# Kernel optimization log

Hardware: AMD Instinct MI355X
Metric: run time of the kernel (lower is better)

## Reference

```python
import jax, jax.numpy as jnp
import numpy as np

H, N, CH = 256, 64, 1

def _r2c(x):
    return x[..., 0] + 1j * x[..., 1]

def setup_inputs() -> dict:
    key = jax.random.key(0)
    kA, kB, kC, kdt = jax.random.split(key, 4)
    # Build a Hurwitz A (skew-Hermitian - 0.5*I) so dA = (I-dt/2 A)^-1 (I+dt/2 A) has spectral radius < 1
    M = jax.random.normal(kA, (H, N, N, 2), dtype=jnp.float32) / np.float32(np.sqrt(N))
    Mc = _r2c(M)
    Ac = 0.5 * (Mc - jnp.conjugate(jnp.swapaxes(Mc, -1, -2))) - 0.5 * jnp.eye(N, dtype=Mc.dtype)
    A = jnp.stack([Ac.real, Ac.imag], axis=-1)  # (H,N,N,2)
    B = jax.random.normal(kB, (H, N, 2), dtype=jnp.float32)
    C = jax.random.normal(kC, (CH, H, N, 2), dtype=jnp.float32)
    # log_dt uniform in [log(1e-3), log(1e-1)], shape (H,1) per bilinear docstring
    log_dt = jax.random.uniform(kdt, (H, 1), dtype=jnp.float32,
                                minval=np.float32(np.log(1e-3)), maxval=np.float32(np.log(1e-1)))
    return {"A": A, "B": B, "C": C, "log_dt": log_dt, "L": 2048}

def _bilinear(dt, Ac, Bc):
    # dt: (H,1), Ac: (H,N,N) complex, Bc: (H,N) complex
    n = Ac.shape[-1]
    I = jnp.eye(n, dtype=Ac.dtype)
    half = (dt.astype(Ac.real.dtype) / 2)[:, None]  # (H,1,1)
    A_back = I - half * Ac
    A_fwd = I + half * Ac
    dB = dt.astype(Ac.dtype) * jnp.linalg.solve(A_back, Bc[..., None])[..., 0]  # (H,N)
    dA = jnp.linalg.solve(A_back, A_fwd)  # (H,N,N)
    return dA, dB

def _krylov(L, dA, dB):
    # x[..., l] = dA^l dB via squaring-doubling, matches S4 krylov math
    x = dB[..., None]  # (H,N,1)
    A_ = dA
    while x.shape[-1] < L:
        x = jnp.concatenate([x, jnp.einsum('hnm,hml->hnl', A_, x)], axis=-1)
        A_ = A_ @ A_
    return x[..., :L]

def reference(A, B, C, log_dt, L):
    Ac, Bc, Cc = _r2c(A), _r2c(B), _r2c(C)
    dt = jnp.exp(log_dt)  # (H,1)
    dA, dB = _bilinear(dt, Ac, Bc)
    x = _krylov(L, dA, dB)  # (H,N,L) complex
    # k[c,h,l] = sum_n C[c,h,n] * (dA^l dB)[h,n]; torch .float() on complex keeps real part
    k = jnp.einsum('chn,hnl->chl', Cc, x).real.astype(jnp.float32)
    return k
```

## Files before the change

kernel.cpp:

```cpp
#include <hip/hip_runtime.h>
#include <math.h>

#define NH   256
#define NN   64
#define LSEQ 2048
#define RS   72
#define PSZ  4608
#define GSZ  2304
#define NTH  1024

typedef __attribute__((ext_vector_type(8))) short short8;
typedef __attribute__((ext_vector_type(4))) float float4_t;
typedef unsigned short u16;

#define MFMA(a,b,c) __builtin_amdgcn_mfma_f32_16x16x32_bf16((a),(b),(c),0,0,0)
#define PERM_HI 0x07060302u

static __device__ __forceinline__ void split2(float v, unsigned& hb, unsigned& lb) {
    hb = __float_as_uint(v) & 0xffff0000u;
    lb = __float_as_uint(v - __uint_as_float(hb));
}
static __device__ __forceinline__ float ld2(const u16* hp, const u16* lp, int idx) {
    return __uint_as_float((unsigned)hp[idx] << 16)
         + __uint_as_float((unsigned)lp[idx] << 16);
}

static __device__ __forceinline__ void frag_vals(const unsigned* e, short8& hi, short8& lo) {
    unsigned lb[8];
#pragma unroll
    for (int m = 0; m < 8; ++m) {
        unsigned hv = e[m] & 0xffff0000u;
        lb[m] = __float_as_uint(__uint_as_float(e[m]) - __uint_as_float(hv));
    }
    union { short8 s; unsigned u[4]; } H, L;
#pragma unroll
    for (int m = 0; m < 4; ++m) {
        H.u[m] = __builtin_amdgcn_perm(e[2*m+1],  e[2*m],  PERM_HI);
        L.u[m] = __builtin_amdgcn_perm(lb[2*m+1], lb[2*m], PERM_HI);
    }
    hi = H.s; lo = L.s;
}

template<int ASZ, int BSZ, bool IMAG>
static __device__ __forceinline__ void cmm_tile(
    const u16* __restrict__ Ab, const u16* __restrict__ Bb,
    int arow, int bcol, int fq,
    float4_t& accP, float4_t& accN, float4_t& accI1, float4_t& accI2)
{
#pragma unroll
    for (int ks = 0; ks < 2; ++ks) {
        const int k0 = ks*32 + fq*8;
        const u16* ap = Ab + arow*RS + k0;
        const u16* bp = Bb + bcol*RS + k0;
        short8 Arh = *(const short8*)(ap);
        short8 Arl = *(const short8*)(ap + ASZ);
        short8 Aih = *(const short8*)(ap + 2*ASZ);
        short8 Ail = *(const short8*)(ap + 3*ASZ);
        short8 Brh = *(const short8*)(bp);
        short8 Brl = *(const short8*)(bp + BSZ);
        short8 Bih = *(const short8*)(bp + 2*BSZ);
        short8 Bil = *(const short8*)(bp + 3*BSZ);
        accP = MFMA(Arh, Brh, accP); accP = MFMA(Arh, Brl, accP); accP = MFMA(Arl, Brh, accP);
        accN = MFMA(Aih, Bih, accN); accN = MFMA(Aih, Bil, accN); accN = MFMA(Ail, Bih, accN);
        if (IMAG) {
            accI1 = MFMA(Arh, Bih, accI1); accI1 = MFMA(Arh, Bil, accI1); accI1 = MFMA(Arl, Bih, accI1);
            accI2 = MFMA(Aih, Brh, accI2); accI2 = MFMA(Aih, Brl, accI2); accI2 = MFMA(Ail, Brh, accI2);
        }
    }
}

static __device__ __forceinline__ void store_P_vals(
    u16* XR, u16* XT, int ti, int bcol, int fq,
    const float* p_r, const float* p_i)
{
    unsigned hR[4], lR[4], hI[4], lI[4];
#pragma unroll
    for (int r = 0; r < 4; ++r) {
        split2(p_r[r], hR[r], lR[r]);
        split2(p_i[r], hI[r], lI[r]);
        int row = ti*16 + fq*4 + r;
        XR[row*RS + bcol]         = (u16)(hR[r] >> 16);
        XR[PSZ + row*RS + bcol]   = (u16)(lR[r] >> 16);
        XR[2*PSZ + row*RS + bcol] = (u16)(hI[r] >> 16);
        XR[3*PSZ + row*RS + bcol] = (u16)(lI[r] >> 16);
    }
    int tb = bcol*RS + ti*16 + fq*4;
    uint2 w;
    w.x = __builtin_amdgcn_perm(hR[1], hR[0], PERM_HI);
    w.y = __builtin_amdgcn_perm(hR[3], hR[2], PERM_HI);
    *(uint2*)&XT[tb] = w;
    w.x = __builtin_amdgcn_perm(lR[1], lR[0], PERM_HI);
    w.y = __builtin_amdgcn_perm(lR[3], lR[2], PERM_HI);
    *(uint2*)&XT[PSZ + tb] = w;
    w.x = __builtin_amdgcn_perm(hI[1], hI[0], PERM_HI);
    w.y = __builtin_amdgcn_perm(hI[3], hI[2], PERM_HI);
    *(uint2*)&XT[2*PSZ + tb] = w;
    w.x = __builtin_amdgcn_perm(lI[1], lI[0], PERM_HI);
    w.y = __builtin_amdgcn_perm(lI[3], lI[2], PERM_HI);
    *(uint2*)&XT[3*PSZ + tb] = w;
}

__global__ __launch_bounds__(NTH, 4) void ssm_kernel(
    const float* __restrict__ Ag,
    const float* __restrict__ Bg,
    const float* __restrict__ Cg,
    const float* __restrict__ LogDt,
    float* __restrict__ outp)
{
    __shared__ __align__(16) unsigned char lds[130048];
    u16* XR = (u16*)(lds);
    u16* XT = (u16*)(lds +  36864);
    u16* XF = (u16*)(lds +  73728);
    u16* Gm = (u16*)(lds + 110592);
    float* bvr = (float*)(lds + 129024);
    float* bvi = (float*)(lds + 129280);
    float* urr = (float*)(lds + 129536);
    float* uri = (float*)(lds + 129792);

    const int t    = threadIdx.x;
    const int lane = t & 63;
    const int wv   = t >> 6;
    const int ti   = wv >> 2, tj = wv & 3;
    const int fm   = lane & 15, fq = lane >> 4;
    const int h    = blockIdx.x;

    const float dt  = expf(LogDt[h]);
    const float hdt = 0.5f * dt;

    const float2* A2 = (const float2*)(Ag + (size_t)h * NN * NN * 2);
    const float4_t z4 = {0.f, 0.f, 0.f, 0.f};

#pragma unroll
    for (int e = 0; e < 4; ++e) {
        int idx = t + e*NTH;
        int i = idx >> 6, j = idx & 63;
        float2 a = A2[idx];
        unsigned hb, lb;
        split2((i == j ? 1.0f : 0.0f) + hdt * a.x, hb, lb);
        XR[i*RS + j]       = (u16)(hb >> 16);
        XR[PSZ + i*RS + j] = (u16)(lb >> 16);
        XT[j*RS + i]       = (u16)(hb >> 16);
        XT[PSZ + j*RS + i] = (u16)(lb >> 16);
        split2(hdt * a.y, hb, lb);
        XR[2*PSZ + i*RS + j] = (u16)(hb >> 16);
        XR[3*PSZ + i*RS + j] = (u16)(lb >> 16);
        XT[2*PSZ + j*RS + i] = (u16)(hb >> 16);
        XT[3*PSZ + j*RS + i] = (u16)(lb >> 16);
    }
    if (t < NN) {
        float2 bv = ((const float2*)Bg)[h*NN + t];
        float2 cv = ((const float2*)Cg)[h*NN + t];
        bvr[t] = bv.x; bvi[t] = bv.y;
        unsigned hb, lb;
        split2(cv.x, hb, lb);
        Gm[t]       = (u16)(hb >> 16);
        Gm[GSZ + t] = (u16)(lb >> 16);
        split2(cv.y, hb, lb);
        Gm[2*GSZ + t] = (u16)(hb >> 16);
        Gm[3*GSZ + t] = (u16)(lb >> 16);
    }
    __syncthreads();

    const int arow = ti*16 + fm;
    const int bcol = tj*16 + fm;

    {
        float4_t aP = z4, aN = z4, aI1 = z4, aI2 = z4;
#pragma unroll
        for (int ks = 0; ks < 2; ++ks) {
            const int k0 = ks*32 + fq*8;
            unsigned vr[8], vi[8];
#pragma unroll
            for (int j = 0; j < 8; ++j) {
                float2 a = A2[arow*NN + k0 + j];
                vr[j] = __float_as_uint((arow == k0 + j ? 1.0f : 0.0f) - hdt * a.x);
                vi[j] = __float_as_uint(-hdt * a.y);
            }
            short8 Arh, Arl, Aih, Ail;
            frag_vals(vr, Arh, Arl);
            frag_vals(vi, Aih, Ail);
            const u16* bp = XT + bcol*RS + k0;
            short8 Brh = *(const short8*)(bp);
            short8 Brl = *(const short8*)(bp + PSZ);
            short8 Bih = *(const short8*)(bp + 2*PSZ);
            short8 Bil = *(const short8*)(bp + 3*PSZ);
            aP = MFMA(Arh, Brh, aP); aP = MFMA(Arh, Brl, aP); aP = MFMA(Arl, Brh, aP);
            aN = MFMA(Aih, Bih, aN); aN = MFMA(Aih, Bil, aN); aN = MFMA(Ail, Bih, aN);
            aI1 = MFMA(Arh, Bih, aI1); aI1 = MFMA(Arh, Bil, aI1); aI1 = MFMA(Arl, Bih, aI1);
            aI2 = MFMA(Aih, Brh, aI2); aI2 = MFMA(Aih, Brl, aI2); aI2 = MFMA(Ail, Brh, aI2);
        }
#pragma unroll
        for (int rp = 0; rp < 2; ++rp) {
            int row0 = ti*16 + fq*4 + rp*2;
            unsigned h0, l0, h1, l1;
            split2(aP[rp*2]   - aN[rp*2],   h0, l0);
            split2(aP[rp*2+1] - aN[rp*2+1], h1, l1);
            *(unsigned*)&XF[bcol*RS + row0]       = __builtin_amdgcn_perm(h1, h0, PERM_HI);
            *(unsigned*)&XF[PSZ + bcol*RS + row0] = __builtin_amdgcn_perm(l1, l0, PERM_HI);
            split2(aI1[rp*2]   + aI2[rp*2],   h0, l0);
            split2(aI1[rp*2+1] + aI2[rp*2+1], h1, l1);
            *(unsigned*)&XF[2*PSZ + bcol*RS + row0] = __builtin_amdgcn_perm(h1, h0, PERM_HI);
            *(unsigned*)&XF[3*PSZ + bcol*RS + row0] = __builtin_amdgcn_perm(l1, l0, PERM_HI);
        }
    }
    __syncthreads();

    {
        float4_t aP = z4, aN = z4, aI1 = z4, aI2 = z4;
        cmm_tile<PSZ, PSZ, true>(XR, XF, arow, bcol, fq, aP, aN, aI1, aI2);
        __syncthreads();
#pragma unroll
        for (int r = 0; r < 4; ++r) {
            int row = ti*16 + fq*4 + r;
            unsigned hb, lb;
            split2(aP[r] - aN[r], hb, lb);
            XR[row*RS + bcol]       = (u16)(hb >> 16);
            XR[PSZ + row*RS + bcol] = (u16)(lb >> 16);
            split2(aI1[r] + aI2[r], hb, lb);
            XR[2*PSZ + row*RS + bcol] = (u16)(hb >> 16);
            XR[3*PSZ + row*RS + bcol] = (u16)(lb >> 16);
        }
    }
    __syncthreads();

    {
        float4_t aP = z4, aN = z4, aI1 = z4, aI2 = z4;
        cmm_tile<PSZ, PSZ, true>(XR, XF, arow, bcol, fq, aP, aN, aI1, aI2);
        float p_r[4], p_i[4];
#pragma unroll
        for (int r = 0; r < 4; ++r) {
            int row = ti*16 + fq*4 + r;
            float2 a = A2[row*NN + bcol];
            float dd  = (row == bcol ? 1.0f : 0.0f);
            float x1r = dd + hdt * a.x;
            float x1i = hdt * a.y;
            float vvr = ld2(XR, XR + PSZ, row*RS + bcol);
            float vvi = ld2(XR + 2*PSZ, XR + 3*PSZ, row*RS + bcol);
            p_r[r] = 2.0f*(3.0f*x1r - 3.0f*vvr + (aP[r] - aN[r])) - dd;
            p_i[r] = 2.0f*(3.0f*x1i - 3.0f*vvi + (aI1[r] + aI2[r]));
        }
        __syncthreads();
        store_P_vals(XR, XT, ti, bcol, fq, p_r, p_i);
    }
    __syncthreads();

    {
        int n = t >> 4, part = t & 15;
        float ar = 0.f, ai = 0.f;
#pragma unroll
        for (int qq = 0; qq < 4; ++qq) {
            int k = part + 16*qq;
            float mr = ld2(XR, XR + PSZ, n*RS + k);
            float mi = ld2(XR + 2*PSZ, XR + 3*PSZ, n*RS + k);
            ar += mr*bvr[k] - mi*bvi[k];
            ai += mr*bvi[k] + mi*bvr[k];
        }
#pragma unroll
        for (int off = 8; off; off >>= 1) { ar += __shfl_xor(ar, off); ai += __shfl_xor(ai, off); }
        if (part == 0) { urr[n] = ar; uri[n] = ai; }
    }
    __syncthreads();

#pragma unroll 1
    for (int s = 1; s <= 9; ++s) {
        if (s == 1) {
            int n = t >> 4, part = t & 15;
            float ar = 0.f, ai = 0.f;
#pragma unroll
            for (int qq = 0; qq < 4; ++qq) {
                int k = part + 16*qq;
                float mr = ld2(XR, XR + PSZ, n*RS + k);
                float mi = ld2(XR + 2*PSZ, XR + 3*PSZ, n*RS + k);
                ar += mr*urr[k] - mi*uri[k];
                ai += mr*uri[k] + mi*urr[k];
            }
#pragma unroll
            for (int off = 8; off; off >>= 1) { ar += __shfl_xor(ar, off); ai += __shfl_xor(ai, off); }
            if (part == 0) {
                float u_r = urr[n], u_i = uri[n];
                unsigned hb, lb;
                split2(hdt*(u_r + bvr[n]), hb, lb);
                XF[n]       = (u16)(hb >> 16); XF[PSZ + n]       = (u16)(lb >> 16);
                split2(hdt*(u_i + bvi[n]), hb, lb);
                XF[2*PSZ + n] = (u16)(hb >> 16); XF[3*PSZ + n]   = (u16)(lb >> 16);
                split2(hdt*(ar + u_r), hb, lb);
                XF[RS + n]       = (u16)(hb >> 16); XF[PSZ + RS + n]   = (u16)(lb >> 16);
                split2(hdt*(ai + u_i), hb, lb);
                XF[2*PSZ + RS + n] = (u16)(hb >> 16); XF[3*PSZ + RS + n] = (u16)(lb >> 16);
            }
        } else if (s <= 6) {
            const int C = 1 << (s-1);
            const int nT = (s == 6) ? 8 : 4;
            if (wv < nT) {
                const int rt = wv >> 2, ct = wv & 3;
                float4_t aP = z4, aN = z4, aI1 = z4, aI2 = z4;
                cmm_tile<PSZ, PSZ, true>(XF, XR, rt*16 + fm, ct*16 + fm, fq, aP, aN, aI1, aI2);
#pragma unroll
                for (int r = 0; r < 4; ++r) {
                    int orow = C + rt*16 + fq*4 + r;
                    int oc   = ct*16 + fm;
                    unsigned hb, lb;
                    split2(aP[r] - aN[r], hb, lb);
                    XF[orow*RS + oc]       = (u16)(hb >> 16);
                    XF[PSZ + orow*RS + oc] = (u16)(lb >> 16);
                    split2(aI1[r] + aI2[r], hb, lb);
                    XF[2*PSZ + orow*RS + oc] = (u16)(hb >> 16);
                    XF[3*PSZ + orow*RS + oc] = (u16)(lb >> 16);
                }
            }
        } else {
            const int C = 1 << (s-7);
            if (wv < 4) {
                float4_t aP = z4, aN = z4, aI1 = z4, aI2 = z4;
                cmm_tile<GSZ, PSZ, true>(Gm, XT, fm, wv*16 + fm, fq, aP, aN, aI1, aI2);
#pragma unroll
                for (int r = 0; r < 4; ++r) {
                    int orow = C + fq*4 + r;
                    int oc   = wv*16 + fm;
                    unsigned hb, lb;
                    split2(aP[r] - aN[r], hb, lb);
                    Gm[orow*RS + oc]       = (u16)(hb >> 16);
                    Gm[GSZ + orow*RS + oc] = (u16)(lb >> 16);
                    split2(aI1[r] + aI2[r], hb, lb);
                    Gm[2*GSZ + orow*RS + oc] = (u16)(hb >> 16);
                    Gm[3*GSZ + orow*RS + oc] = (u16)(lb >> 16);
                }
            }
        }
        float4_t sP = z4, sN = z4, sI1 = z4, sI2 = z4;
        cmm_tile<PSZ, PSZ, true>(XR, XT, arow, bcol, fq, sP, sN, sI1, sI2);
        __syncthreads();
        float p_r[4], p_i[4];
#pragma unroll
        for (int r = 0; r < 4; ++r) { p_r[r] = sP[r] - sN[r]; p_i[r] = sI1[r] + sI2[r]; }
        store_P_vals(XR, XT, ti, bcol, fq, p_r, p_i);
        __syncthreads();
    }

#pragma unroll 1
    for (int tt = 0; tt < 4; ++tt) {
        if (tt < 3 && wv < 4) {
            const int ab = tt * 8;
            float4_t aP = z4, aN = z4, aI1 = z4, aI2 = z4;
            cmm_tile<GSZ, PSZ, true>(Gm, XT, ab + fm, wv*16 + fm, fq, aP, aN, aI1, aI2);
#pragma unroll
            for (int r = 0; r < 4; ++r) {
                int orow = 8 + ab + fq*4 + r;
                if (orow < 32) {
                    int oc = wv*16 + fm;
                    unsigned hb, lb;
                    split2(aP[r] - aN[r], hb, lb);
                    Gm[orow*RS + oc]       = (u16)(hb >> 16);
                    Gm[GSZ + orow*RS + oc] = (u16)(lb >> 16);
                    split2(aI1[r] + aI2[r], hb, lb);
                    Gm[2*GSZ + orow*RS + oc] = (u16)(hb >> 16);
                    Gm[3*GSZ + orow*RS + oc] = (u16)(lb >> 16);
                }
            }
        }
        if (wv >= 4 && wv < 8) {
            const int jb = tt * 8;
            int ga = jb + fm; if (ga > 31) ga = 31;
            float4_t aP = z4, aN = z4, aI1 = z4, aI2 = z4;
            cmm_tile<GSZ, PSZ, false>(Gm, XF, ga, (wv-4)*16 + fm, fq, aP, aN, aI1, aI2);
            if (fq < 2) {
                size_t base = (size_t)h * LSEQ;
#pragma unroll
                for (int r = 0; r < 4; ++r)
                    outp[base + (jb + fq*4 + r)*NN + (wv-4)*16 + fm] = aP[r] - aN[r];
            }
        }
        if (tt < 3) __syncthreads();
    }
}

extern "C" void kernel_launch(void* const* d_in, const int* in_sizes, int n_in,
                              void* d_out, int out_size, void* d_ws, size_t ws_size,
                              hipStream_t stream) {
    const float* A  = (const float*)d_in[0];
    const float* B  = (const float*)d_in[1];
    const float* C  = (const float*)d_in[2];
    const float* ld = (const float*)d_in[3];
    float* out = (float*)d_out;
    ssm_kernel<<<dim3(NH), dim3(NTH), 0, stream>>>(A, B, C, ld, out);
}
```

Baseline: 99.89 us.

## Split waves: half compute paired squaring tiles, half run Krylov steps concurrently

The 64x64 complex matrix squaring now uses only waves 0-7, each computing two 16x16 output tiles that share the A fragment, instead of all 16 waves computing one tile each. Waves 8-15 take over the Krylov extension and Gm work and run it concurrently with the squaring rather than serially before it. The aim is to reuse A-operand LDS loads and overlap the two independent chains inside each step. In exchange each squaring wave has twice the work and uses more accumulator registers, and the diff leaves in a dead dummy load.

```diff
diff --git a/kernel.cpp b/kernel.cpp
--- a/kernel.cpp
+++ b/kernel.cpp
@@ -69,6 +69,51 @@
     }
 }
 
+template<int ASZ, int BSZ>
+static __device__ __forceinline__ void cmm_pair(
+    const u16* __restrict__ Ab, const u16* __restrict__ Bb,
+    int arow, int bcol0, int fq,
+    float4_t& P0, float4_t& N0, float4_t& I10, float4_t& I20,
+    float4_t& P1, float4_t& N1, float4_t& I11, float4_t& I21)
+{
+#pragma unroll
+    for (int ks = 0; ks < 2; ++ks) {
+        const int k0 = ks*32 + fq*8;
+        const u16* ap = Ab + arow*RS + k0;
+        short8 Arh = *(const short8*)(ap);
+        short8 Arl = *(const short8*)(ap + ASZ);
+        short8 Aih = *(const short8*)(ap + 2*ASZ);
+        short8 Ail = *(const short8*)(ap + 3*ASZ);
+        const u16* bp0 = Bb + bcol0*RS + k0;
+        {
+            short8 Brh = *(const short8*)(bp0);
+            short8 Brl = *(const short8*)(bp0 + BSZ);
+            short8 Bih = *(const short8*)(bp0 + 2*BSZ);
+            short8 Bil = *(const short8*)(bp0 + 3*BSZ);
+            P0 = MFMA(Arh, Brh, P0); P0 = MFMA(Arh, Brl, P0); P0 = MFMA(Arl, Brh, P0);
+            N0 = MFMA(Aih, Bih, N0); N0 = MFMA(Aih, Bil, N0); N0 = MFMA(Ail, Bih, N0);
+            I10 = MFMA(Arh, Bih, I10); I10 = MFMA(Arh, Bil, I10); I10 = MFMA(Arl, Bih, I10);
+            I20 = MFMA(Aih, Brh, I20); I20 = MFMA(Aih, Brl, I20); I20 = MFMA(Ail, Brh, I20);
+        }
+        {
+            const u16* bp1 = bp0 + 16;
+            short8 Brh = *(const short8*)(bp1 + 16*(RS/16)*0 + (RS*16 - 16) + 16 - RS*16 + RS*16);
+            (void)Brh;
+        }
+        {
+            const u16* bp1 = Bb + (bcol0 + 16)*RS + k0;
+            short8 Brh = *(const short8*)(bp1);
+            short8 Brl = *(const short8*)(bp1 + BSZ);
+            short8 Bih = *(const short8*)(bp1 + 2*BSZ);
+            short8 Bil = *(const short8*)(bp1 + 3*BSZ);
+            P1 = MFMA(Arh, Brh, P1); P1 = MFMA(Arh, Brl, P1); P1 = MFMA(Arl, Brh, P1);
+            N1 = MFMA(Aih, Bih, N1); N1 = MFMA(Aih, Bil, N1); N1 = MFMA(Ail, Bih, N1);
+            I11 = MFMA(Arh, Bih, I11); I11 = MFMA(Arh, Bil, I11); I11 = MFMA(Arl, Bih, I11);
+            I21 = MFMA(Aih, Brh, I21); I21 = MFMA(Aih, Brl, I21); I21 = MFMA(Ail, Brh, I21);
+        }
+    }
+}
+
 static __device__ __forceinline__ void store_P_vals(
     u16* XR, u16* XT, int ti, int bcol, int fq,
     const float* p_r, const float* p_i)
@@ -120,9 +165,13 @@
     const int t    = threadIdx.x;
     const int lane = t & 63;
     const int wv   = t >> 6;
-    const int ti   = wv >> 2, tj = wv & 3;
     const int fm   = lane & 15, fq = lane >> 4;
     const int h    = blockIdx.x;
+
+    const int tip  = wv >> 1, tjp = wv & 1;
+    const int parow = tip*16 + fm;
+    const int pb0   = tjp*32 + fm;
+    const int pb1   = pb0 + 16;
 
     const float dt  = expf(LogDt[h]);
     const float hdt = 0.5f * dt;
@@ -161,86 +210,117 @@
     }
     __syncthreads();
 
-    const int arow = ti*16 + fm;
-    const int bcol = tj*16 + fm;
-
-    {
-        float4_t aP = z4, aN = z4, aI1 = z4, aI2 = z4;
+    if (wv < 8) {
+        float4_t P0 = z4, N0 = z4, I10 = z4, I20 = z4;
+        float4_t P1 = z4, N1 = z4, I11 = z4, I21 = z4;
 #pragma unroll
         for (int ks = 0; ks < 2; ++ks) {
             const int k0 = ks*32 + fq*8;
             unsigned vr[8], vi[8];
 #pragma unroll
             for (int j = 0; j < 8; ++j) {
-                float2 a = A2[arow*NN + k0 + j];
-                vr[j] = __float_as_uint((arow == k0 + j ? 1.0f : 0.0f) - hdt * a.x);
+                float2 a = A2[parow*NN + k0 + j];
+                vr[j] = __float_as_uint((parow == k0 + j ? 1.0f : 0.0f) - hdt * a.x);
                 vi[j] = __float_as_uint(-hdt * a.y);
             }
             short8 Arh, Arl, Aih, Ail;
             frag_vals(vr, Arh, Arl);
             frag_vals(vi, Aih, Ail);
-            const u16* bp = XT + bcol*RS + k0;
-            short8 Brh = *(const short8*)(bp);
-            short8 Brl = *(const short8*)(bp + PSZ);
-            short8 Bih = *(const short8*)(bp + 2*PSZ);
-            short8 Bil = *(const short8*)(bp + 3*PSZ);
-            aP = MFMA(Arh, Brh, aP); aP = MFMA(Arh, Brl, aP); aP = MFMA(Arl, Brh, aP);
-            aN = MFMA(Aih, Bih, aN); aN = MFMA(Aih, Bil, aN); aN = MFMA(Ail, Bih, aN);
-            aI1 = MFMA(Arh, Bih, aI1); aI1 = MFMA(Arh, Bil, aI1); aI1 = MFMA(Arl, Bih, aI1);
-            aI2 = MFMA(Aih, Brh, aI2); aI2 = MFMA(Aih, Brl, aI2); aI2 = MFMA(Ail, Brh, aI2);
-        }
-#pragma unroll
-        for (int rp = 0; rp < 2; ++rp) {
-            int row0 = ti*16 + fq*4 + rp*2;
-            unsigned h0, l0, h1, l1;
-            split2(aP[rp*2]   - aN[rp*2],   h0, l0);
-            split2(aP[rp*2+1] - aN[rp*2+1], h1, l1);
-            *(unsigned*)&XF[bcol*RS + row0]       = __builtin_amdgcn_perm(h1, h0, PERM_HI);
-            *(unsigned*)&XF[PSZ + bcol*RS + row0] = __builtin_amdgcn_perm(l1, l0, PERM_HI);
-            split2(aI1[rp*2]   + aI2[rp*2],   h0, l0);
-            split2(aI1[rp*2+1] + aI2[rp*2+1], h1, l1);
-            *(unsigned*)&XF[2*PSZ + bcol*RS + row0] = __builtin_amdgcn_perm(h1, h0, PERM_HI);
-            *(unsigned*)&XF[3*PSZ + bcol*RS + row0] = __builtin_amdgcn_perm(l1, l0, PERM_HI);
+#pragma unroll
+            for (int p = 0; p < 2; ++p) {
+                const u16* bp = XT + (pb0 + p*16)*RS + k0;
+                short8 Brh = *(const short8*)(bp);
+                short8 Brl = *(const short8*)(bp + PSZ);
+                short8 Bih = *(const short8*)(bp + 2*PSZ);
+                short8 Bil = *(const short8*)(bp + 3*PSZ);
+                float4_t &aP = p ? P1 : P0, &aN = p ? N1 : N0;
+                float4_t &aI1 = p ? I11 : I10, &aI2 = p ? I21 : I20;
+                aP = MFMA(Arh, Brh, aP); aP = MFMA(Arh, Brl, aP); aP = MFMA(Arl, Brh, aP);
+                aN = MFMA(Aih, Bih, aN); aN = MFMA(Aih, Bil, aN); aN = MFMA(Ail, Bih, aN);
+                aI1 = MFMA(Arh, Bih, aI1); aI1 = MFMA(Arh, Bil, aI1); aI1 = MFMA(Arl, Bih, aI1);
+                aI2 = MFMA(Aih, Brh, aI2); aI2 = MFMA(Aih, Brl, aI2); aI2 = MFMA(Ail, Brh, aI2);
+            }
+        }
+#pragma unroll
+        for (int p = 0; p < 2; ++p) {
+            const int bcol = pb0 + p*16;
+            const float4_t &aP = p ? P1 : P0, &aN = p ? N1 : N0;
+            const float4_t &aI1 = p ? I11 : I10, &aI2 = p ? I21 : I20;
+#pragma unroll
+            for (int rp = 0; rp < 2; ++rp) {
+                int row0 = tip*16 + fq*4 + rp*2;
+                unsigned h0, l0, h1, l1;
+                split2(aP[rp*2]   - aN[rp*2],   h0, l0);
+                split2(aP[rp*2+1] - aN[rp*2+1], h1, l1);
+                *(unsigned*)&XF[bcol*RS + row0]       = __builtin_amdgcn_perm(h1, h0, PERM_HI);
+                *(unsigned*)&XF[PSZ + bcol*RS + row0] = __builtin_amdgcn_perm(l1, l0, PERM_HI);
+                split2(aI1[rp*2]   + aI2[rp*2],   h0, l0);
+                split2(aI1[rp*2+1] + aI2[rp*2+1], h1, l1);
+                *(unsigned*)&XF[2*PSZ + bcol*RS + row0] = __builtin_amdgcn_perm(h1, h0, PERM_HI);
+                *(unsigned*)&XF[3*PSZ + bcol*RS + row0] = __builtin_amdgcn_perm(l1, l0, PERM_HI);
+            }
         }
     }
     __syncthreads();
 
     {
-        float4_t aP = z4, aN = z4, aI1 = z4, aI2 = z4;
-        cmm_tile<PSZ, PSZ, true>(XR, XF, arow, bcol, fq, aP, aN, aI1, aI2);
+        float4_t P0 = z4, N0 = z4, I10 = z4, I20 = z4;
+        float4_t P1 = z4, N1 = z4, I11 = z4, I21 = z4;
+        if (wv < 8)
+            cmm_pair<PSZ, PSZ>(XR, XF, parow, pb0, fq, P0, N0, I10, I20, P1, N1, I11, I21);
         __syncthreads();
-#pragma unroll
-        for (int r = 0; r < 4; ++r) {
-            int row = ti*16 + fq*4 + r;
-            unsigned hb, lb;
-            split2(aP[r] - aN[r], hb, lb);
-            XR[row*RS + bcol]       = (u16)(hb >> 16);
-            XR[PSZ + row*RS + bcol] = (u16)(lb >> 16);
-            split2(aI1[r] + aI2[r], hb, lb);
-            XR[2*PSZ + row*RS + bcol] = (u16)(hb >> 16);
-            XR[3*PSZ + row*RS + bcol] = (u16)(lb >> 16);
+        if (wv < 8) {
+#pragma unroll
+            for (int p = 0; p < 2; ++p) {
+                const int bcol = pb0 + p*16;
+                const float4_t &aP = p ? P1 : P0, &aN = p ? N1 : N0;
+                const float4_t &aI1 = p ? I11 : I10, &aI2 = p ? I21 : I20;
+#pragma unroll
+                for (int r = 0; r < 4; ++r) {
+                    int row = tip*16 + fq*4 + r;
+                    unsigned hb, lb;
+                    split2(aP[r] - aN[r], hb, lb);
+                    XR[row*RS + bcol]       = (u16)(hb >> 16);
+                    XR[PSZ + row*RS + bcol] = (u16)(lb >> 16);
+                    split2(aI1[r] + aI2[r], hb, lb);
+                    XR[2*PSZ + row*RS + bcol] = (u16)(hb >> 16);
+                    XR[3*PSZ + row*RS + bcol] = (u16)(lb >> 16);
+                }
+            }
         }
     }
     __syncthreads();
 
     {
-        float4_t aP = z4, aN = z4, aI1 = z4, aI2 = z4;
-        cmm_tile<PSZ, PSZ, true>(XR, XF, arow, bcol, fq, aP, aN, aI1, aI2);
-        float p_r[4], p_i[4];
-#pragma unroll
-        for (int r = 0; r < 4; ++r) {
-            int row = ti*16 + fq*4 + r;
-            float2 a = A2[row*NN + bcol];
-            float dd  = (row == bcol ? 1.0f : 0.0f);
-            float x1r = dd + hdt * a.x;
-            float x1i = hdt * a.y;
-            float vvr = ld2(XR, XR + PSZ, row*RS + bcol);
-            float vvi = ld2(XR + 2*PSZ, XR + 3*PSZ, row*RS + bcol);
-            p_r[r] = 2.0f*(3.0f*x1r - 3.0f*vvr + (aP[r] - aN[r])) - dd;
-            p_i[r] = 2.0f*(3.0f*x1i - 3.0f*vvi + (aI1[r] + aI2[r]));
+        float p_r[2][4], p_i[2][4];
+        if (wv < 8) {
+            float4_t P0 = z4, N0 = z4, I10 = z4, I20 = z4;
+            float4_t P1 = z4, N1 = z4, I11 = z4, I21 = z4;
+            cmm_pair<PSZ, PSZ>(XR, XF, parow, pb0, fq, P0, N0, I10, I20, P1, N1, I11, I21);
+#pragma unroll
+            for (int p = 0; p < 2; ++p) {
+                const int bcol = pb0 + p*16;
+                const float4_t &aP = p ? P1 : P0, &aN = p ? N1 : N0;
+                const float4_t &aI1 = p ? I11 : I10, &aI2 = p ? I21 : I20;
+#pragma unroll
+                for (int r = 0; r < 4; ++r) {
+                    int row = tip*16 + fq*4 + r;
+                    float2 a = A2[row*NN + bcol];
+                    float dd  = (row == bcol ? 1.0f : 0.0f);
+                    float x1r = dd + hdt * a.x;
+                    float x1i = hdt * a.y;
+                    float vvr = ld2(XR, XR + PSZ, row*RS + bcol);
+                    float vvi = ld2(XR + 2*PSZ, XR + 3*PSZ, row*RS + bcol);
+                    p_r[p][r] = 2.0f*(3.0f*x1r - 3.0f*vvr + (aP[r] - aN[r])) - dd;
+                    p_i[p][r] = 2.0f*(3.0f*x1i - 3.0f*vvi + (aI1[r] + aI2[r]));
+                }
+            }
         }
         __syncthreads();
-        store_P_vals(XR, XT, ti, bcol, fq, p_r, p_i);
+        if (wv < 8) {
+            store_P_vals(XR, XT, tip, pb0, fq, p_r[0], p_i[0]);
+            store_P_vals(XR, XT, tip, pb1, fq, p_r[1], p_i[1]);
+        }
     }
     __syncthreads();
 
@@ -263,77 +343,88 @@
 
 #pragma unroll 1
     for (int s = 1; s <= 9; ++s) {
-        if (s == 1) {
-            int n = t >> 4, part = t & 15;
-            float ar = 0.f, ai = 0.f;
-#pragma unroll
-            for (int qq = 0; qq < 4; ++qq) {
-                int k = part + 16*qq;
-                float mr = ld2(XR, XR + PSZ, n*RS + k);
-                float mi = ld2(XR + 2*PSZ, XR + 3*PSZ, n*RS + k);
-                ar += mr*urr[k] - mi*uri[k];
-                ai += mr*uri[k] + mi*urr[k];
-            }
-#pragma unroll
-            for (int off = 8; off; off >>= 1) { ar += __shfl_xor(ar, off); ai += __shfl_xor(ai, off); }
-            if (part == 0) {
-                float u_r = urr[n], u_i = uri[n];
-                unsigned hb, lb;
-                split2(hdt*(u_r + bvr[n]), hb, lb);
-                XF[n]       = (u16)(hb >> 16); XF[PSZ + n]       = (u16)(lb >> 16);
-                split2(hdt*(u_i + bvi[n]), hb, lb);
-                XF[2*PSZ + n] = (u16)(hb >> 16); XF[3*PSZ + n]   = (u16)(lb >> 16);
-                split2(hdt*(ar + u_r), hb, lb);
-                XF[RS + n]       = (u16)(hb >> 16); XF[PSZ + RS + n]   = (u16)(lb >> 16);
-                split2(hdt*(ai + u_i), hb, lb);
-                XF[2*PSZ + RS + n] = (u16)(hb >> 16); XF[3*PSZ + RS + n] = (u16)(lb >> 16);
-            }
-        } else if (s <= 6) {
-            const int C = 1 << (s-1);
-            const int nT = (s == 6) ? 8 : 4;
-            if (wv < nT) {
-                const int rt = wv >> 2, ct = wv & 3;
-                float4_t aP = z4, aN = z4, aI1 = z4, aI2 = z4;
-                cmm_tile<PSZ, PSZ, true>(XF, XR, rt*16 + fm, ct*16 + fm, fq, aP, aN, aI1, aI2);
-#pragma unroll
-                for (int r = 0; r < 4; ++r) {
-                    int orow = C + rt*16 + fq*4 + r;
-                    int oc   = ct*16 + fm;
+        float4_t P0 = z4, N0 = z4, I10 = z4, I20 = z4;
+        float4_t P1 = z4, N1 = z4, I11 = z4, I21 = z4;
+        if (wv >= 8) {
+            if (s == 1) {
+                int n = (t >> 3) & 63, part = t & 7;
+                float ar = 0.f, ai = 0.f;
+#pragma unroll
+                for (int qq = 0; qq < 8; ++qq) {
+                    int k = part + 8*qq;
+                    float mr = ld2(XR, XR + PSZ, n*RS + k);
+                    float mi = ld2(XR + 2*PSZ, XR + 3*PSZ, n*RS + k);
+                    ar += mr*urr[k] - mi*uri[k];
+                    ai += mr*uri[k] + mi*urr[k];
+                }
+#pragma unroll
+                for (int off = 4; off; off >>= 1) { ar += __shfl_xor(ar, off); ai += __shfl_xor(ai, off); }
+                if (part == 0) {
+                    float u_r = urr[n], u_i = uri[n];
                     unsigned hb, lb;
-                    split2(aP[r] - aN[r], hb, lb);
-                    XF[orow*RS + oc]       = (u16)(hb >> 16);
-                    XF[PSZ + orow*RS + oc] = (u16)(lb >> 16);
-                    split2(aI1[r] + aI2[r], hb, lb);
-                    XF[2*PSZ + orow*RS + oc] = (u16)(hb >> 16);
-                    XF[3*PSZ + orow*RS + oc] = (u16)(lb >> 16);
+                    split2(hdt*(u_r + bvr[n]), hb, lb);
+                    XF[n]       = (u16)(hb >> 16); XF[PSZ + n]       = (u16)(lb >> 16);
+                    split2(hdt*(u_i + bvi[n]), hb, lb);
+                    XF[2*PSZ + n] = (u16)(hb >> 16); XF[3*PSZ + n]   = (u16)(lb >> 16);
+                    split2(hdt*(ar + u_r), hb, lb);
+                    XF[RS + n]       = (u16)(hb >> 16); XF[PSZ + RS + n]   = (u16)(lb >> 16);
+                    split2(hdt*(ai + u_i), hb, lb);
+                    XF[2*PSZ + RS + n] = (u16)(hb >> 16); XF[3*PSZ + RS + n] = (u16)(lb >> 16);
+                }
+            } else if (s <= 6) {
+                const int C = 1 << (s-1);
+                const int w = wv - 8;
+                const int nT = (s == 6) ? 8 : 4;
+                if (w < nT) {
+                    const int rt = w >> 2, ct = w & 3;
+                    float4_t aP = z4, aN = z4, aI1 = z4, aI2 = z4;
+                    cmm_tile<PSZ, PSZ, true>(XF, XR, rt*16 + fm, ct*16 + fm, fq, aP, aN, aI1, aI2);
+#pragma unroll
+                    for (int r = 0; r < 4; ++r) {
+                        int orow = C + rt*16 + fq*4 + r;
+                        int oc   = ct*16 + fm;
+                        unsigned hb, lb;
+                        split2(aP[r] - aN[r], hb, lb);
+                        XF[orow*RS + oc]       = (u16)(hb >> 16);
+                        XF[PSZ + orow*RS + oc] = (u16)(lb >> 16);
+                        split2(aI1[r] + aI2[r], hb, lb);
+                        XF[2*PSZ + orow*RS + oc] = (u16)(hb >> 16);
+                        XF[3*PSZ + orow*RS + oc] = (u16)(lb >> 16);
+                    }
+                }
+            } else {
+                const int C = 1 << (s-7);
+                const int w = wv - 8;
+                if (w < 4) {
+                    float4_t aP = z4, aN = z4, aI1 = z4, aI2 = z4;
+                    cmm_tile<GSZ, PSZ, true>(Gm, XT, fm, w*16 + fm, fq, aP, aN, aI1, aI2);
+#pragma unroll
+                    for (int r = 0; r < 4; ++r) {
+                        int orow = C + fq*4 + r;
+                        int oc   = w*16 + fm;
+                        unsigned hb, lb;
+                        split2(aP[r] - aN[r], hb, lb);
+                        Gm[orow*RS + oc]       = (u16)(hb >> 16);
+                        Gm[GSZ + orow*RS + oc] = (u16)(lb >> 16);
+                        split2(aI1[r] + aI2[r], hb, lb);
+                        Gm[2*GSZ + orow*RS + oc] = (u16)(hb >> 16);
+                        Gm[3*GSZ + orow*RS + oc] = (u16)(lb >> 16);
+                    }
                 }
             }
         } else {
-            const int C = 1 << (s-7);
-            if (wv < 4) {
-                float4_t aP = z4, aN = z4, aI1 = z4, aI2 = z4;
-                cmm_tile<GSZ, PSZ, true>(Gm, XT, fm, wv*16 + fm, fq, aP, aN, aI1, aI2);
-#pragma unroll
-                for (int r = 0; r < 4; ++r) {
-                    int orow = C + fq*4 + r;
-                    int oc   = wv*16 + fm;
-                    unsigned hb, lb;
-                    split2(aP[r] - aN[r], hb, lb);
-                    Gm[orow*RS + oc]       = (u16)(hb >> 16);
-                    Gm[GSZ + orow*RS + oc] = (u16)(lb >> 16);
-                    split2(aI1[r] + aI2[r], hb, lb);
-                    Gm[2*GSZ + orow*RS + oc] = (u16)(hb >> 16);
-                    Gm[3*GSZ + orow*RS + oc] = (u16)(lb >> 16);
-                }
-            }
-        }
-        float4_t sP = z4, sN = z4, sI1 = z4, sI2 = z4;
-        cmm_tile<PSZ, PSZ, true>(XR, XT, arow, bcol, fq, sP, sN, sI1, sI2);
+            cmm_pair<PSZ, PSZ>(XR, XT, parow, pb0, fq, P0, N0, I10, I20, P1, N1, I11, I21);
+        }
         __syncthreads();
-        float p_r[4], p_i[4];
-#pragma unroll
-        for (int r = 0; r < 4; ++r) { p_r[r] = sP[r] - sN[r]; p_i[r] = sI1[r] + sI2[r]; }
-        store_P_vals(XR, XT, ti, bcol, fq, p_r, p_i);
+        if (wv < 8) {
+            float p_r[4], p_i[4];
+#pragma unroll
+            for (int r = 0; r < 4; ++r) { p_r[r] = P0[r] - N0[r]; p_i[r] = I10[r] + I20[r]; }
+            store_P_vals(XR, XT, tip, pb0, fq, p_r, p_i);
+#pragma unroll
+            for (int r = 0; r < 4; ++r) { p_r[r] = P1[r] - N1[r]; p_i[r] = I11[r] + I21[r]; }
+            store_P_vals(XR, XT, tip, pb1, fq, p_r, p_i);
+        }
         __syncthreads();
     }
 
```

After: 97.21 us. 1.03x faster.
